# Kernel tuning notes

Measured on AMD Instinct MI355X. Metric: run time of the kernel, lower is better.

## Reference

```python
import jax, jax.numpy as jnp
import numpy as np

VAR_EPS = 1e-6
N, HID = 100000, 512
D, PH = 64, 16  # input_size, prep_hidden
NOBS = 50000


def setup_inputs() -> dict:
    key = jax.random.key(0)
    ks = jax.random.split(key, 10)
    std = np.sqrt(2.0 / (4 + PH))
    k_gru = 1.0 / np.sqrt(HID)
    inp = {
        "h": jax.random.normal(ks[0], (N, HID), jnp.float32),
        "p": jax.random.normal(ks[1], (N, 2 * D), jnp.float32),
        "X_obs": jax.random.normal(ks[2], (NOBS, D), jnp.float32),
        "M_obs": (jax.random.uniform(ks[3], (NOBS, D)) < 0.5).astype(jnp.float32),
        "i_obs": jnp.sort(jax.random.randint(ks[4], (NOBS,), 0, N)),
        "w_prep": std * jax.random.normal(ks[5], (D, 4, PH), jnp.float32),
        "bias_prep": 0.1 + jnp.zeros((D, PH), jnp.float32),
        "weight_ih": jax.random.uniform(ks[6], (3 * HID, PH * D), jnp.float32, -k_gru, k_gru),
        "weight_hh": jax.random.uniform(ks[7], (3 * HID, HID), jnp.float32, -k_gru, k_gru),
        "bias_ih": jax.random.uniform(ks[8], (3 * HID,), jnp.float32, -k_gru, k_gru),
        "bias_hh": jax.random.uniform(ks[9], (3 * HID,), jnp.float32, -k_gru, k_gru),
    }
    return inp


def _gru_cell(x, hprev, Wih, Whh, bih, bhh):
    gi = x @ Wih.T + bih            # [n, 3H]
    gh = hprev @ Whh.T + bhh        # [n, 3H]
    ir, iz, inn = jnp.split(gi, 3, axis=1)
    hr, hz, hn = jnp.split(gh, 3, axis=1)
    r = jax.nn.sigmoid(ir + hr)
    z = jax.nn.sigmoid(iz + hz)
    n = jnp.tanh(inn + r * hn)
    return (1.0 - z) * n + z * hprev


def reference(h, p, X_obs, M_obs, i_obs, w_prep, bias_prep, weight_ih, weight_hh, bias_ih, bias_hh):
    p_obs = p[i_obs]                              # [n, 2D] gather
    mean, var = jnp.split(p_obs, 2, axis=1)
    var = jnp.abs(var) + VAR_EPS
    error = (X_obs - mean) / jnp.sqrt(var)
    loss = 0.5 * jnp.sum((error * error + jnp.log(var)) * M_obs)

    feats = jnp.stack([X_obs, mean, var, error], axis=2)   # [n, D, 4]
    gru_in = jnp.einsum('ndf,dfp->ndp', feats, w_prep) + bias_prep  # [n, D, PH]
    gru_in = jax.nn.relu(gru_in) * M_obs[:, :, None]
    gru_in = gru_in.reshape(-1, D * PH)

    h_obs_new = _gru_cell(gru_in, h[i_obs], weight_ih, weight_hh, bias_ih, bias_hh)
    h_new = h.at[i_obs].set(h_obs_new)
    return h_new, loss
```

## Files before the change

kernel.cpp:

```cpp
#include <hip/hip_runtime.h>
#include <math.h>

#define NHID 512
typedef unsigned short u16;
typedef __attribute__((ext_vector_type(8))) short short8;
typedef __attribute__((ext_vector_type(16))) float floatx16;

__device__ __forceinline__ unsigned f2b1(float f) {
  unsigned u = __float_as_uint(f);
  return (u + 0x7FFFu + ((u >> 16) & 1u)) >> 16;
}
__device__ __forceinline__ unsigned pk2(float a, float b) {
  return f2b1(a) | (f2b1(b) << 16);
}
__device__ __forceinline__ float sigf(float x) { return 1.0f / (1.0f + expf(-x)); }

__global__ void wtransform(const float* __restrict__ W, uint4* __restrict__ Wt,
                           int Kw, int nch) {
  int u = blockIdx.x * 256 + threadIdx.x;
  int total = 8 * 3 * nch * 512;
  if (u >= total) return;
  int col = u & 63;
  int g8 = (u >> 6) & 7;
  int ch = (u >> 9) % nch;
  int t3 = (u >> 9) / nch;
  int g = t3 % 3, cbb = t3 / 3;
  const float* src = W + (size_t)(g * 512 + cbb * 64 + col) * Kw + ch * 64 + g8 * 8;
  float4 f0 = *(const float4*)src;
  float4 f1 = *(const float4*)(src + 4);
  uint4 v = {pk2(f0.x, f0.y), pk2(f0.z, f0.w), pk2(f1.x, f1.y), pk2(f1.z, f1.w)};
  Wt[u] = v;
}

__global__ void prep_kernel(const float* __restrict__ p,
                            const float* __restrict__ X,
                            const float* __restrict__ Mm,
                            const int* __restrict__ iobs,
                            const float* __restrict__ wprep,
                            const float* __restrict__ bprep,
                            const float* __restrict__ h,
                            u16* __restrict__ A_in, u16* __restrict__ A_h,
                            int* __restrict__ map_i, int* __restrict__ counter,
                            float* __restrict__ partials, int nobs)
{
  __shared__ float sw[4096];
  __shared__ float sb[1024];
  __shared__ int s_cnt[4];
  __shared__ float s_loss[4];
  for (int t = threadIdx.x; t < 4096; t += 256) sw[t] = wprep[t];
  for (int t = threadIdx.x; t < 1024; t += 256) sb[t] = bprep[t];

  const int tid = threadIdx.x;
  const int wave = tid >> 6;
  const int d = tid & 63;
  const int j = blockIdx.x * 4 + wave;
  const bool act = j < nobs;

  int i = 0; bool lastf = false;
  float x = 0.f, mean = 0.f, var = 1.f, m = 0.f, err = 0.f, lossp = 0.f;
  if (act) {
    i = iobs[j];
    lastf = (j == nobs - 1) || (iobs[j + 1] != i);
    mean = p[(size_t)i * 128 + d];
    var  = fabsf(p[(size_t)i * 128 + 64 + d]) + 1e-6f;
    x = X[(size_t)j * 64 + d];
    m = Mm[(size_t)j * 64 + d];
    err = (x - mean) * rsqrtf(var);
    lossp = 0.5f * (err * err + logf(var)) * m;
  }
  __syncthreads();

  #pragma unroll
  for (int off = 32; off > 0; off >>= 1) lossp += __shfl_down(lossp, off, 64);
  if (d == 0) { s_loss[wave] = lossp; s_cnt[wave] = (act && lastf) ? 1 : 0; }
  __syncthreads();
  if (tid == 0) {
    int c0 = s_cnt[0], c1 = s_cnt[1], c2 = s_cnt[2], c3 = s_cnt[3];
    int tot = c0 + c1 + c2 + c3;
    int base = tot ? atomicAdd(counter, tot) : 0;
    s_cnt[0] = base; s_cnt[1] = base + c0;
    s_cnt[2] = base + c0 + c1; s_cnt[3] = base + c0 + c1 + c2;
    partials[blockIdx.x] = s_loss[0] + s_loss[1] + s_loss[2] + s_loss[3];
  }
  __syncthreads();

  if (act && lastf) {
    const int slot = s_cnt[wave];
    if (d == 0) map_i[slot] = i;
    const float* w = sw + d * 64;
    const float* b = sb + d * 16;
    float gi[16];
    #pragma unroll
    for (int ph = 0; ph < 16; ++ph) {
      float v = x * w[ph] + mean * w[16 + ph] + var * w[32 + ph] + err * w[48 + ph] + b[ph];
      gi[ph] = fmaxf(v, 0.0f) * m;
    }
    uint4* dst = (uint4*)(A_in + (size_t)slot * 1024 + d * 16);
    uint4 v0 = {pk2(gi[0], gi[1]), pk2(gi[2], gi[3]), pk2(gi[4], gi[5]), pk2(gi[6], gi[7])};
    uint4 v1 = {pk2(gi[8], gi[9]), pk2(gi[10], gi[11]), pk2(gi[12], gi[13]), pk2(gi[14], gi[15])};
    dst[0] = v0; dst[1] = v1;
    const float4* hp = (const float4*)(h + (size_t)i * NHID + d * 8);
    float4 a = hp[0], bb = hp[1];
    uint4 hv = {pk2(a.x, a.y), pk2(a.z, a.w), pk2(bb.x, bb.y), pk2(bb.z, bb.w)};
    *(uint4*)(A_h + (size_t)slot * 512 + d * 8) = hv;
  }
}

__global__ void loss_sum(const float* __restrict__ partials, int n,
                         float* __restrict__ loss) {
  float s = 0.f;
  for (int t = threadIdx.x; t < n; t += 256) s += partials[t];
  #pragma unroll
  for (int off = 32; off > 0; off >>= 1) s += __shfl_down(s, off, 64);
  __shared__ float sw4[4];
  if ((threadIdx.x & 63) == 0) sw4[threadIdx.x >> 6] = s;
  __syncthreads();
  if (threadIdx.x == 0) loss[0] = sw4[0] + sw4[1] + sw4[2] + sw4[3];
}

__global__ __launch_bounds__(256, 4) void gemm_mfma(
    const u16* __restrict__ A_in, const u16* __restrict__ A_h,
    const uint4* __restrict__ Wt_ih, const uint4* __restrict__ Wt_hh,
    const int* __restrict__ map_i, const int* __restrict__ counter,
    const float* __restrict__ h,
    const float* __restrict__ bih, const float* __restrict__ bhh,
    float* __restrict__ out)
{
  const int ndist = *counter;
  const int j0 = blockIdx.y * 64;
  if (j0 >= ndist) return;
  const int cb = blockIdx.x;
  const int tid = threadIdx.x;
  const int lane = tid & 63;
  const int wave = tid >> 6;
  const int wrow = wave >> 1, wcol = wave & 1;
  const int l31 = lane & 31, kh = lane >> 5;

  __shared__ uint4 sA[8 * 64];
  __shared__ uint4 sB[3 * 8 * 64];

  floatx16 accR = {}, accZ = {}, accI = {}, accH = {};

#define STAGE(Asrc, Ks, Wt, NCH, ch)                                         \
  {                                                                          \
    _Pragma("unroll") for (int pp = 0; pp < 2; ++pp) {                       \
      int g8 = (tid >> 6) + pp * 4;                                          \
      int row = tid & 63;                                                    \
      int gr = j0 + row; if (gr >= ndist) gr = ndist - 1;                    \
      sA[g8 * 64 + row] =                                                    \
          *(const uint4*)(Asrc + (size_t)gr * Ks + ch * 64 + g8 * 8);        \
    }                                                                        \
    _Pragma("unroll") for (int pp = 0; pp < 6; ++pp) {                       \
      int idx = pp * 256 + tid;                                              \
      int g = idx >> 9, rem = idx & 511;                                     \
      sB[idx] = Wt[(size_t)((cb * 3 + g) * NCH + ch) * 512 + rem];           \
    }                                                                        \
  }

#define KSTEPS(ACC3)                                                         \
  _Pragma("unroll") for (int s = 0; s < 4; ++s) {                            \
    int u = (s * 2 + kh) * 64;                                               \
    uint4 av = sA[u + l31 + 32 * wrow];                                      \
    uint4 b0 = sB[0 * 512 + u + l31 + 32 * wcol];                            \
    uint4 b1 = sB[1 * 512 + u + l31 + 32 * wcol];                            \
    uint4 b2 = sB[2 * 512 + u + l31 + 32 * wcol];                            \
    short8 aF = __builtin_bit_cast(short8, av);                              \
    short8 f0 = __builtin_bit_cast(short8, b0);                              \
    short8 f1 = __builtin_bit_cast(short8, b1);                              \
    short8 f2 = __builtin_bit_cast(short8, b2);                              \
    accR = __builtin_amdgcn_mfma_f32_32x32x16_bf16(aF, f0, accR, 0, 0, 0);   \
    accZ = __builtin_amdgcn_mfma_f32_32x32x16_bf16(aF, f1, accZ, 0, 0, 0);   \
    ACC3 = __builtin_amdgcn_mfma_f32_32x32x16_bf16(aF, f2, ACC3, 0, 0, 0);   \
  }

  for (int ch = 0; ch < 16; ++ch) {
    STAGE(A_in, 1024, Wt_ih, 16, ch)
    __syncthreads();
    KSTEPS(accI)
    __syncthreads();
  }
  for (int ch = 0; ch < 8; ++ch) {
    STAGE(A_h, 512, Wt_hh, 8, ch)
    __syncthreads();
    KSTEPS(accH)
    __syncthreads();
  }

  const int col = cb * 64 + 32 * wcol + l31;
  const float biR = bih[col], biZ = bih[512 + col], biN = bih[1024 + col];
  const float bhR = bhh[col], bhZ = bhh[512 + col], bhN = bhh[1024 + col];
  #pragma unroll
  for (int r = 0; r < 16; ++r) {
    int rowl = (r & 3) + 8 * (r >> 2) + 4 * kh + 32 * wrow;
    int jg = j0 + rowl;
    if (jg >= ndist) continue;
    int i = map_i[jg];
    float hv = h[(size_t)i * NHID + col];
    float rr = sigf(accR[r] + biR + bhR);
    float zz = sigf(accZ[r] + biZ + bhZ);
    float nn = tanhf(accI[r] + biN + rr * (accH[r] + bhN));
    out[(size_t)i * NHID + col] = (1.0f - zz) * nn + zz * hv;
  }
#undef STAGE
#undef KSTEPS
}

extern "C" void kernel_launch(void* const* d_in, const int* in_sizes, int n_in,
                              void* d_out, int out_size, void* d_ws, size_t ws_size,
                              hipStream_t stream) {
  const float* h     = (const float*)d_in[0];
  const float* p     = (const float*)d_in[1];
  const float* X     = (const float*)d_in[2];
  const float* Mm    = (const float*)d_in[3];
  const int*   iobs  = (const int*)d_in[4];
  const float* wprep = (const float*)d_in[5];
  const float* bprep = (const float*)d_in[6];
  const float* Wih   = (const float*)d_in[7];
  const float* Whh   = (const float*)d_in[8];
  const float* bih   = (const float*)d_in[9];
  const float* bhh   = (const float*)d_in[10];

  const int N    = in_sizes[0] / NHID;
  const int nobs = in_sizes[4];
  float* out = (float*)d_out;
  float* loss = out + (size_t)N * NHID;

  char* ws = (char*)d_ws;
  int*   counter  = (int*)ws;
  int*   map_i    = (int*)(ws + 1024);
  float* partials = (float*)(ws + (256 << 10));
  u16*   A_in     = (u16*)(ws + (1 << 20));
  u16*   A_h      = (u16*)((char*)A_in + (size_t)nobs * 2048);
  uint4* Wt_ih    = (uint4*)((char*)A_h + (size_t)nobs * 1024);
  uint4* Wt_hh    = (uint4*)((char*)Wt_ih + (size_t)3145728);

  hipMemcpyAsync(d_out, d_in[0], (size_t)N * NHID * sizeof(float),
                 hipMemcpyDeviceToDevice, stream);
  hipMemsetAsync(counter, 0, 4, stream);

  wtransform<<<768, 256, 0, stream>>>(Wih, Wt_ih, 1024, 16);
  wtransform<<<384, 256, 0, stream>>>(Whh, Wt_hh, 512, 8);

  int nblocks = (nobs + 3) / 4;
  prep_kernel<<<nblocks, 256, 0, stream>>>(p, X, Mm, iobs, wprep, bprep, h,
                                           A_in, A_h, map_i, counter, partials, nobs);
  loss_sum<<<1, 256, 0, stream>>>(partials, nblocks, loss);

  dim3 grid(8, (nobs + 63) / 64);
  gemm_mfma<<<grid, 256, 0, stream>>>(A_in, A_h, Wt_ih, Wt_hh, map_i, counter,
                                      h, bih, bhh, out);
}
```

Baseline: 934.8 us.

## Fuse setup launches, pre-tile GEMM operands, and drop LDS staging in GRU GEMM

Merges the weight transforms, the counter reset and the h-to-out copy into one housekeeping kernel, and folds the loss reduction into block 0 of the GEMM. This removes the memcpy, memset and extra launches. The prep kernel now writes A and H tiles in an MFMA fragment-major layout, so the GEMM reads fragments straight from global memory with no shared-memory staging or barriers. It also remaps block indices for L2 locality and lowers launch bounds to 3 waves per SIMD. Dropping LDS staging risks redundant global or L2 traffic and exposed load latency, since nothing prefetches ahead.

```diff
diff --git a/kernel.cpp b/kernel.cpp
--- a/kernel.cpp
+++ b/kernel.cpp
@@ -15,11 +15,9 @@
 }
 __device__ __forceinline__ float sigf(float x) { return 1.0f / (1.0f + expf(-x)); }
 
-__global__ void wtransform(const float* __restrict__ W, uint4* __restrict__ Wt,
-                           int Kw, int nch) {
-  int u = blockIdx.x * 256 + threadIdx.x;
-  int total = 8 * 3 * nch * 512;
-  if (u >= total) return;
+__device__ __forceinline__ void wt_body(const float* __restrict__ W,
+                                        uint4* __restrict__ Wt, int Kw,
+                                        int nch, int u) {
   int col = u & 63;
   int g8 = (u >> 6) & 7;
   int ch = (u >> 9) % nch;
@@ -32,6 +30,27 @@
   Wt[u] = v;
 }
 
+__global__ void housekeeping(const float* __restrict__ Wih, uint4* __restrict__ Wt_ih,
+                             const float* __restrict__ Whh, uint4* __restrict__ Wt_hh,
+                             const float4* __restrict__ h4, float4* __restrict__ out4,
+                             int n4, int* __restrict__ counter) {
+  int b = blockIdx.x;
+  if (b < 768) {
+    wt_body(Wih, Wt_ih, 1024, 16, b * 256 + (int)threadIdx.x);
+    return;
+  }
+  if (b < 1152) {
+    wt_body(Whh, Wt_hh, 512, 8, (b - 768) * 256 + (int)threadIdx.x);
+    return;
+  }
+  if (b == 1152) {
+    if (threadIdx.x == 0) *counter = 0;
+    return;
+  }
+  int i = (b - 1153) * 256 + threadIdx.x;
+  for (; i < n4; i += 2048 * 256) out4[i] = h4[i];
+}
+
 __global__ void prep_kernel(const float* __restrict__ p,
                             const float* __restrict__ X,
                             const float* __restrict__ Mm,
@@ -39,7 +58,7 @@
                             const float* __restrict__ wprep,
                             const float* __restrict__ bprep,
                             const float* __restrict__ h,
-                            u16* __restrict__ A_in, u16* __restrict__ A_h,
+                            uint4* __restrict__ A_fm, uint4* __restrict__ H_fm,
                             int* __restrict__ map_i, int* __restrict__ counter,
                             float* __restrict__ partials, int nobs)
 {
@@ -87,6 +106,7 @@
   if (act && lastf) {
     const int slot = s_cnt[wave];
     if (d == 0) map_i[slot] = i;
+    const int g = slot >> 6, row = slot & 63;
     const float* w = sw + d * 64;
     const float* b = sb + d * 16;
     float gi[16];
@@ -95,95 +115,93 @@
       float v = x * w[ph] + mean * w[16 + ph] + var * w[32 + ph] + err * w[48 + ph] + b[ph];
       gi[ph] = fmaxf(v, 0.0f) * m;
     }
-    uint4* dst = (uint4*)(A_in + (size_t)slot * 1024 + d * 16);
     uint4 v0 = {pk2(gi[0], gi[1]), pk2(gi[2], gi[3]), pk2(gi[4], gi[5]), pk2(gi[6], gi[7])};
     uint4 v1 = {pk2(gi[8], gi[9]), pk2(gi[10], gi[11]), pk2(gi[12], gi[13]), pk2(gi[14], gi[15])};
-    dst[0] = v0; dst[1] = v1;
+    uint4* fmA = A_fm + ((size_t)((g * 16 + (d >> 2)) * 8 + (d & 3) * 2)) * 64 + row;
+    fmA[0]  = v0;
+    fmA[64] = v1;
     const float4* hp = (const float4*)(h + (size_t)i * NHID + d * 8);
     float4 a = hp[0], bb = hp[1];
     uint4 hv = {pk2(a.x, a.y), pk2(a.z, a.w), pk2(bb.x, bb.y), pk2(bb.z, bb.w)};
-    *(uint4*)(A_h + (size_t)slot * 512 + d * 8) = hv;
-  }
-}
-
-__global__ void loss_sum(const float* __restrict__ partials, int n,
-                         float* __restrict__ loss) {
-  float s = 0.f;
-  for (int t = threadIdx.x; t < n; t += 256) s += partials[t];
-  #pragma unroll
-  for (int off = 32; off > 0; off >>= 1) s += __shfl_down(s, off, 64);
-  __shared__ float sw4[4];
-  if ((threadIdx.x & 63) == 0) sw4[threadIdx.x >> 6] = s;
-  __syncthreads();
-  if (threadIdx.x == 0) loss[0] = sw4[0] + sw4[1] + sw4[2] + sw4[3];
-}
-
-__global__ __launch_bounds__(256, 4) void gemm_mfma(
-    const u16* __restrict__ A_in, const u16* __restrict__ A_h,
+    H_fm[((size_t)((g * 8 + (d >> 3)) * 8 + (d & 7))) * 64 + row] = hv;
+  }
+}
+
+__global__ __launch_bounds__(256, 3) void gemm_mfma(
+    const uint4* __restrict__ A_fm, const uint4* __restrict__ H_fm,
     const uint4* __restrict__ Wt_ih, const uint4* __restrict__ Wt_hh,
     const int* __restrict__ map_i, const int* __restrict__ counter,
     const float* __restrict__ h,
     const float* __restrict__ bih, const float* __restrict__ bhh,
-    float* __restrict__ out)
+    const float* __restrict__ partials, int nparts,
+    float* __restrict__ out, float* __restrict__ loss)
 {
+  const int tid = threadIdx.x;
+  if (blockIdx.x == 0) {
+    float s = 0.f;
+    for (int t = tid; t < nparts; t += 256) s += partials[t];
+    #pragma unroll
+    for (int off = 32; off > 0; off >>= 1) s += __shfl_down(s, off, 64);
+    __shared__ float sw4[4];
+    if ((tid & 63) == 0) sw4[tid >> 6] = s;
+    __syncthreads();
+    if (tid == 0) loss[0] = sw4[0] + sw4[1] + sw4[2] + sw4[3];
+    return;
+  }
+
   const int ndist = *counter;
-  const int j0 = blockIdx.y * 64;
+  const int bid = blockIdx.x - 1;
+  const int jb = (bid & 7) + 8 * (bid >> 6);
+  const int cb = (bid >> 3) & 7;
+  const int j0 = jb * 64;
   if (j0 >= ndist) return;
-  const int cb = blockIdx.x;
-  const int tid = threadIdx.x;
+
   const int lane = tid & 63;
   const int wave = tid >> 6;
   const int wrow = wave >> 1, wcol = wave & 1;
   const int l31 = lane & 31, kh = lane >> 5;
-
-  __shared__ uint4 sA[8 * 64];
-  __shared__ uint4 sB[3 * 8 * 64];
+  const int arow = l31 + 32 * wrow;
+  const int bcol = l31 + 32 * wcol;
 
   floatx16 accR = {}, accZ = {}, accI = {}, accH = {};
 
-#define STAGE(Asrc, Ks, Wt, NCH, ch)                                         \
-  {                                                                          \
-    _Pragma("unroll") for (int pp = 0; pp < 2; ++pp) {                       \
-      int g8 = (tid >> 6) + pp * 4;                                          \
-      int row = tid & 63;                                                    \
-      int gr = j0 + row; if (gr >= ndist) gr = ndist - 1;                    \
-      sA[g8 * 64 + row] =                                                    \
-          *(const uint4*)(Asrc + (size_t)gr * Ks + ch * 64 + g8 * 8);        \
-    }                                                                        \
-    _Pragma("unroll") for (int pp = 0; pp < 6; ++pp) {                       \
-      int idx = pp * 256 + tid;                                              \
-      int g = idx >> 9, rem = idx & 511;                                     \
-      sB[idx] = Wt[(size_t)((cb * 3 + g) * NCH + ch) * 512 + rem];           \
-    }                                                                        \
-  }
-
-#define KSTEPS(ACC3)                                                         \
-  _Pragma("unroll") for (int s = 0; s < 4; ++s) {                            \
-    int u = (s * 2 + kh) * 64;                                               \
-    uint4 av = sA[u + l31 + 32 * wrow];                                      \
-    uint4 b0 = sB[0 * 512 + u + l31 + 32 * wcol];                            \
-    uint4 b1 = sB[1 * 512 + u + l31 + 32 * wcol];                            \
-    uint4 b2 = sB[2 * 512 + u + l31 + 32 * wcol];                            \
-    short8 aF = __builtin_bit_cast(short8, av);                              \
-    short8 f0 = __builtin_bit_cast(short8, b0);                              \
-    short8 f1 = __builtin_bit_cast(short8, b1);                              \
-    short8 f2 = __builtin_bit_cast(short8, b2);                              \
-    accR = __builtin_amdgcn_mfma_f32_32x32x16_bf16(aF, f0, accR, 0, 0, 0);   \
-    accZ = __builtin_amdgcn_mfma_f32_32x32x16_bf16(aF, f1, accZ, 0, 0, 0);   \
-    ACC3 = __builtin_amdgcn_mfma_f32_32x32x16_bf16(aF, f2, ACC3, 0, 0, 0);   \
-  }
-
-  for (int ch = 0; ch < 16; ++ch) {
-    STAGE(A_in, 1024, Wt_ih, 16, ch)
-    __syncthreads();
-    KSTEPS(accI)
-    __syncthreads();
-  }
-  for (int ch = 0; ch < 8; ++ch) {
-    STAGE(A_h, 512, Wt_hh, 8, ch)
-    __syncthreads();
-    KSTEPS(accH)
-    __syncthreads();
+  for (int cl = 0; cl < 16; ++cl) {
+    const uint4* Ap = A_fm + (size_t)(jb * 16 + cl) * 512;
+    const uint4* Bp = Wt_ih + (size_t)(cb * 48 + cl) * 512;
+    #pragma unroll
+    for (int s = 0; s < 4; ++s) {
+      int u = (s * 2 + kh) * 64;
+      uint4 av = Ap[u + arow];
+      uint4 b0 = Bp[u + bcol];
+      uint4 b1 = Bp[8192 + u + bcol];
+      uint4 b2 = Bp[16384 + u + bcol];
+      short8 aF = __builtin_bit_cast(short8, av);
+      accR = __builtin_amdgcn_mfma_f32_32x32x16_bf16(
+          aF, __builtin_bit_cast(short8, b0), accR, 0, 0, 0);
+      accZ = __builtin_amdgcn_mfma_f32_32x32x16_bf16(
+          aF, __builtin_bit_cast(short8, b1), accZ, 0, 0, 0);
+      accI = __builtin_amdgcn_mfma_f32_32x32x16_bf16(
+          aF, __builtin_bit_cast(short8, b2), accI, 0, 0, 0);
+    }
+  }
+  for (int cl = 0; cl < 8; ++cl) {
+    const uint4* Ap = H_fm + (size_t)(jb * 8 + cl) * 512;
+    const uint4* Bp = Wt_hh + (size_t)(cb * 24 + cl) * 512;
+    #pragma unroll
+    for (int s = 0; s < 4; ++s) {
+      int u = (s * 2 + kh) * 64;
+      uint4 av = Ap[u + arow];
+      uint4 b0 = Bp[u + bcol];
+      uint4 b1 = Bp[4096 + u + bcol];
+      uint4 b2 = Bp[8192 + u + bcol];
+      short8 aF = __builtin_bit_cast(short8, av);
+      accR = __builtin_amdgcn_mfma_f32_32x32x16_bf16(
+          aF, __builtin_bit_cast(short8, b0), accR, 0, 0, 0);
+      accZ = __builtin_amdgcn_mfma_f32_32x32x16_bf16(
+          aF, __builtin_bit_cast(short8, b1), accZ, 0, 0, 0);
+      accH = __builtin_amdgcn_mfma_f32_32x32x16_bf16(
+          aF, __builtin_bit_cast(short8, b2), accH, 0, 0, 0);
+    }
   }
 
   const int col = cb * 64 + 32 * wcol + l31;
@@ -201,8 +219,6 @@
     float nn = tanhf(accI[r] + biN + rr * (accH[r] + bhN));
     out[(size_t)i * NHID + col] = (1.0f - zz) * nn + zz * hv;
   }
-#undef STAGE
-#undef KSTEPS
 }
 
 extern "C" void kernel_launch(void* const* d_in, const int* in_sizes, int n_in,
@@ -225,28 +241,27 @@
   float* out = (float*)d_out;
   float* loss = out + (size_t)N * NHID;
 
+  const int ngmax = (nobs + 63) / 64;
+
   char* ws = (char*)d_ws;
   int*   counter  = (int*)ws;
   int*   map_i    = (int*)(ws + 1024);
   float* partials = (float*)(ws + (256 << 10));
-  u16*   A_in     = (u16*)(ws + (1 << 20));
-  u16*   A_h      = (u16*)((char*)A_in + (size_t)nobs * 2048);
-  uint4* Wt_ih    = (uint4*)((char*)A_h + (size_t)nobs * 1024);
+  uint4* A_fm     = (uint4*)(ws + (1 << 20));
+  uint4* H_fm     = (uint4*)((char*)A_fm + (size_t)ngmax * 131072);
+  uint4* Wt_ih    = (uint4*)((char*)H_fm + (size_t)ngmax * 65536);
   uint4* Wt_hh    = (uint4*)((char*)Wt_ih + (size_t)3145728);
 
-  hipMemcpyAsync(d_out, d_in[0], (size_t)N * NHID * sizeof(float),
-                 hipMemcpyDeviceToDevice, stream);
-  hipMemsetAsync(counter, 0, 4, stream);
-
-  wtransform<<<768, 256, 0, stream>>>(Wih, Wt_ih, 1024, 16);
-  wtransform<<<384, 256, 0, stream>>>(Whh, Wt_hh, 512, 8);
+  housekeeping<<<3201, 256, 0, stream>>>(Wih, Wt_ih, Whh, Wt_hh,
+                                         (const float4*)h, (float4*)out,
+                                         N * 128, counter);
 
   int nblocks = (nobs + 3) / 4;
   prep_kernel<<<nblocks, 256, 0, stream>>>(p, X, Mm, iobs, wprep, bprep, h,
-                                           A_in, A_h, map_i, counter, partials, nobs);
-  loss_sum<<<1, 256, 0, stream>>>(partials, nblocks, loss);
-
-  dim3 grid(8, (nobs + 63) / 64);
-  gemm_mfma<<<grid, 256, 0, stream>>>(A_in, A_h, Wt_ih, Wt_hh, map_i, counter,
-                                      h, bih, bhh, out);
-}
+                                           A_fm, H_fm, map_i, counter, partials, nobs);
+
+  int nhi = (ngmax + 7) / 8;
+  gemm_mfma<<<1 + 64 * nhi, 256, 0, stream>>>(A_fm, H_fm, Wt_ih, Wt_hh, map_i,
+                                              counter, h, bih, bhh,
+                                              partials, nblocks, out, loss);
+}
```

Result: faster. 914.6 us (-2.2%).
